# Kernel tuning notes

Measured on AMD Instinct MI355X. Metric: run time of the kernel, lower is better.

Reference implementation:

```python
import jax, jax.numpy as jnp
import numpy as np

B, F, E, A, T, H = 16384, 1024, 28, 2, 128, 4
HD = T // H  # head dim = 32

def _ln(x, g, b, eps=1e-5):
    m = jnp.mean(x, axis=-1, keepdims=True)
    v = jnp.var(x, axis=-1, keepdims=True)
    return (x - m) / jnp.sqrt(v + eps) * g + b

def _gelu(x):
    return jax.nn.gelu(x, approximate=False)  # torch nn.GELU default (erf)

def setup_inputs() -> dict:
    key = jax.random.key(0)
    ks = iter(jax.random.split(key, 48))
    def rn(shape, s=0.02):
        return jax.random.normal(next(ks), shape, jnp.float32) * s
    d = dict(
        fusion_feat=jax.random.normal(next(ks), (B, F), jnp.float32),
        explicit_logits=jax.random.normal(next(ks), (B, E), jnp.float32),
        implicit_logits=jax.random.normal(next(ks), (B, E), jnp.float32),
        affect_vec=jax.random.normal(next(ks), (B, A), jnp.float32),
        ln_exp_g=jnp.ones((E,), jnp.float32), ln_exp_b=jnp.zeros((E,), jnp.float32),
        W_exp=rn((E, T)), b_exp=jnp.zeros((T,), jnp.float32),
        ln_imp_g=jnp.ones((E,), jnp.float32), ln_imp_b=jnp.zeros((E,), jnp.float32),
        W_imp=rn((E, T)), b_imp=jnp.zeros((T,), jnp.float32),
        ln_aff_g=jnp.ones((A,), jnp.float32), ln_aff_b=jnp.zeros((A,), jnp.float32),
        W_aff=rn((A, T)), b_aff=jnp.zeros((T,), jnp.float32),
        Wq_in=rn((F, T)), bq_in=jnp.zeros((T,), jnp.float32),   # query_proj
        Wq=rn((T, T)), bq=jnp.zeros((T,), jnp.float32),         # MHA in_proj q
        Wk=rn((T, T)), bk=jnp.zeros((T,), jnp.float32),         # MHA in_proj k
        Wv=rn((T, T)), bv=jnp.zeros((T,), jnp.float32),         # MHA in_proj v
        Wo=rn((T, T)), bo=jnp.zeros((T,), jnp.float32),         # MHA out_proj
        Wc=rn((T, F)), bc=jnp.zeros((F,), jnp.float32),         # context_proj
        Ws=rn((3 * T, F)), bs=jnp.zeros((F,), jnp.float32),     # summary_proj
        Wg1=rn((2 * F, F)), bg1=jnp.zeros((F,), jnp.float32),   # gate layer 1
        Wg2=rn((F, F)), bg2=jnp.zeros((F,), jnp.float32),       # gate layer 2
        ln_out_g=jnp.ones((F,), jnp.float32), ln_out_b=jnp.zeros((F,), jnp.float32),
    )
    return d

def reference(fusion_feat, explicit_logits, implicit_logits, affect_vec,
              ln_exp_g, ln_exp_b, W_exp, b_exp,
              ln_imp_g, ln_imp_b, W_imp, b_imp,
              ln_aff_g, ln_aff_b, W_aff, b_aff,
              Wq_in, bq_in, Wq, bq, Wk, bk, Wv, bv, Wo, bo,
              Wc, bc, Ws, bs, Wg1, bg1, Wg2, bg2, ln_out_g, ln_out_b):
    p_exp = jax.nn.softmax(explicit_logits, axis=-1)
    p_imp = jax.nn.softmax(implicit_logits, axis=-1)
    exp_e = _gelu(_ln(p_exp, ln_exp_g, ln_exp_b) @ W_exp + b_exp)       # (B,T)
    imp_e = _gelu(_ln(p_imp, ln_imp_g, ln_imp_b) @ W_imp + b_imp)       # (B,T)
    aff_e = _gelu(_ln(affect_vec, ln_aff_g, ln_aff_b) @ W_aff + b_aff)  # (B,T)
    tokens = jnp.stack([exp_e, imp_e, aff_e], axis=1)                   # (B,3,T)
    q = fusion_feat @ Wq_in + bq_in                                     # (B,T)
    # tiny 1-query x 3-key multi-head cross attention (dropout=eval/identity)
    qh = (q @ Wq + bq).reshape(B, H, HD)
    kh = (tokens @ Wk + bk).reshape(B, 3, H, HD)
    vh = (tokens @ Wv + bv).reshape(B, 3, H, HD)
    scores = jnp.einsum('bhd,bshd->bhs', qh, kh) / np.float32(np.sqrt(HD))
    w = jax.nn.softmax(scores, axis=-1)                                 # (B,H,3)
    attn_weights = jnp.mean(w, axis=1)                                  # avg heads -> (B,3)
    attn_out = jnp.einsum('bhs,bshd->bhd', w, vh).reshape(B, T) @ Wo + bo
    context = attn_out @ Wc + bc                                        # (B,F)
    gate_h = _gelu(jnp.concatenate([fusion_feat, context], axis=-1) @ Wg1 + bg1)
    gate = jax.nn.sigmoid(gate_h @ Wg2 + bg2)
    refined = _ln(fusion_feat + gate * context, ln_out_g, ln_out_b)
    summary = _gelu(jnp.concatenate([exp_e, imp_e, aff_e], axis=-1) @ Ws + bs)
    return refined, attn_weights, summary
```

## Files before the change

### kernel.cpp

```cpp
#include <hip/hip_runtime.h>
#include <hip/hip_bf16.h>
#include <stdint.h>


using bf16 = __hip_bfloat16;
typedef __bf16 bf16x8 __attribute__((ext_vector_type(8)));
typedef float f32x4 __attribute__((ext_vector_type(4)));

__device__ __forceinline__ float b2f(bf16 x) { return __bfloat162float(x); }
__device__ __forceinline__ bf16 f2b(float x) { return __float2bfloat16(x); }

__device__ __forceinline__ float fast_tanh(float y) {
  float z = fabsf(y);
  float t = __expf(-2.f * z);
  float r = (1.f - t) / (1.f + t);
  return copysignf(r, y);
}
__device__ __forceinline__ float gelu_f(float x) {
  return 0.5f * x * (1.f + fast_tanh(0.7978845608028654f * (x + 0.044715f * x * x * x)));
}
__device__ __forceinline__ float sigmoid_f(float v) {
  return 1.f / (1.f + __expf(-v));
}

__device__ __forceinline__ void async_ld16(const void* g, void* l) {
  using GP = const __attribute__((address_space(1))) uint32_t*;
  using LP = __attribute__((address_space(3))) uint32_t*;
  __builtin_amdgcn_global_load_lds((GP)g, (LP)l, 16, 0, 0);
}

template <int EPI, typename OutT, int MT>
__device__ __forceinline__ void gemm128_dev(
    int bx, int by,
    const bf16* A0, const bf16* A1, int ksplit, int lda0, int lda1,
    const bf16* __restrict__ BT, int K,
    const float* __restrict__ bias,
    OutT* out, int ldo,
    const bf16* ffp, const bf16* ctxp, int ldfc)
{
  constexpr int MIC = MT / 32;
  __shared__ uint16_t smA[MT * 64];
  __shared__ uint16_t smB[128 * 64];
  const int tid = threadIdx.x;
  const int w = tid >> 6;
  const int l = tid & 63;
  const int m0 = bx * MT;
  const int n0 = by * 128;
  const int wr = w >> 1, wc = w & 1;
  const int lrow = l & 15, lquad = l >> 4;
  const int rb = w * 8 + (l >> 3);
  const int cpos = l & 7;

  const f32x4 vzero = {0.f, 0.f, 0.f, 0.f};
  f32x4 acc[MIC][4];
#pragma unroll
  for (int i = 0; i < MIC; i++)
#pragma unroll
    for (int j = 0; j < 4; j++) acc[i][j] = vzero;

  for (int k0 = 0; k0 < K; k0 += 64) {
    __syncthreads();
#pragma unroll
    for (int i = 0; i < MIC; i++) {
      int row = i * 32 + rb;
      int cg = cpos ^ (row & 7);
      int kcol = k0 + cg * 8;
      const bf16* gp = (kcol < ksplit)
                           ? (A0 + (size_t)(m0 + row) * lda0 + kcol)
                           : (A1 + (size_t)(m0 + row) * lda1 + (kcol - ksplit));
      async_ld16(gp, &smA[(i * 32 + w * 8) * 64]);
    }
#pragma unroll
    for (int i = 0; i < 4; i++) {
      int row = i * 32 + rb;
      int cg = cpos ^ (row & 7);
      const bf16* gq = BT + (size_t)(n0 + row) * K + k0 + cg * 8;
      async_ld16(gq, &smB[(i * 32 + w * 8) * 64]);
    }
    __syncthreads();
#pragma unroll
    for (int kk = 0; kk < 2; kk++) {
      bf16x8 af[MIC], bfr[4];
      const int cc = kk * 4 + lquad;
#pragma unroll
      for (int mi = 0; mi < MIC; mi++) {
        int r = wr * (MT / 2) + mi * 16 + lrow;
        af[mi] = *(const bf16x8*)&smA[r * 64 + ((cc ^ (r & 7)) << 3)];
      }
#pragma unroll
      for (int ni = 0; ni < 4; ni++) {
        int r = wc * 64 + ni * 16 + lrow;
        bfr[ni] = *(const bf16x8*)&smB[r * 64 + ((cc ^ (r & 7)) << 3)];
      }
#pragma unroll
      for (int mi = 0; mi < MIC; mi++)
#pragma unroll
        for (int ni = 0; ni < 4; ni++)
          acc[mi][ni] =
              __builtin_amdgcn_mfma_f32_16x16x32_bf16(af[mi], bfr[ni], acc[mi][ni], 0, 0, 0);
    }
  }

#pragma unroll
  for (int mi = 0; mi < MIC; mi++) {
#pragma unroll
    for (int ni = 0; ni < 4; ni++) {
#pragma unroll
      for (int r = 0; r < 4; r++) {
        int row = m0 + wr * (MT / 2) + mi * 16 + lquad * 4 + r;
        int col = n0 + wc * 64 + ni * 16 + lrow;
        float v = acc[mi][ni][r] + (bias ? bias[col] : 0.f);
        if (EPI == 1) v = gelu_f(v);
        if (EPI == 2) {
          float gate = sigmoid_f(v);
          size_t fo = (size_t)row * ldfc + col;
          v = b2f(ffp[fo]) + gate * b2f(ctxp[fo]);
        }
        if constexpr (__is_same(OutT, float))
          out[(size_t)row * ldo + col] = v;
        else
          out[(size_t)row * ldo + col] = f2b(v);
      }
    }
  }
}

template <int EPI, typename OutT>
__device__ __forceinline__ void gemm256_dev(
    uint16_t* __restrict__ smem, int bx, int by,
    const bf16* A0, const bf16* A1, int ksplit, int lda0, int lda1,
    const bf16* B0, const bf16* B1, int bsplit, int ldb0, int ldb1,
    int K,
    const float* __restrict__ bias,
    OutT* out, int ldo,
    const bf16* ffp, const bf16* ctxp, int ldfc)
{
  const int tid = threadIdx.x;
  const int w = tid >> 6;
  const int l = tid & 63;
  const int m0 = bx * 256;
  const int n0 = by * 256;
  const int wr = w >> 2;
  const int wc = w & 3;
  const int lrow = l & 15, lquad = l >> 4;
  const int rb = tid >> 3;
  const int cpos = tid & 7;
  const int NT = K >> 6;

  const f32x4 vzero = {0.f, 0.f, 0.f, 0.f};
  f32x4 acc[8][4];
#pragma unroll
  for (int mi = 0; mi < 8; mi++)
#pragma unroll
    for (int ni = 0; ni < 4; ni++) acc[mi][ni] = vzero;

  auto stage = [&](int buf, int tt) {
    const int k0 = tt << 6;
    const bf16* Ab; int la, kc;
    if (k0 < ksplit) { Ab = A0; la = lda0; kc = k0; }
    else             { Ab = A1; la = lda1; kc = k0 - ksplit; }
    uint16_t* sA = smem + buf * 16384;
#pragma unroll
    for (int i = 0; i < 4; i++) {
      const int row = i * 64 + rb;
      const int cg = cpos ^ (row & 7);
      async_ld16(Ab + (size_t)(m0 + row) * la + kc + cg * 8,
                 &sA[(i * 64 + w * 8) * 64]);
    }
    const bf16* Bb; int lb, kb;
    if (k0 < bsplit) { Bb = B0; lb = ldb0; kb = k0; }
    else             { Bb = B1; lb = ldb1; kb = k0 - bsplit; }
    uint16_t* sB = smem + 32768 + buf * 16384;
#pragma unroll
    for (int i = 0; i < 4; i++) {
      const int row = i * 64 + rb;
      const int cg = cpos ^ (row & 7);
      async_ld16(Bb + (size_t)(n0 + row) * lb + kb + cg * 8,
                 &sB[(i * 64 + w * 8) * 64]);
    }
  };

  int cur = 0;

  auto readfrags = [&](int kk, bf16x8 (&af)[8], bf16x8 (&bfr)[4]) {
    const uint16_t* sA = smem + cur * 16384;
    const uint16_t* sB = smem + 32768 + cur * 16384;
    const int cc = kk * 4 + lquad;
#pragma unroll
    for (int mi = 0; mi < 8; mi++) {
      int r = wr * 128 + mi * 16 + lrow;
      af[mi] = *(const bf16x8*)&sA[r * 64 + ((cc ^ (r & 7)) << 3)];
    }
#pragma unroll
    for (int ni = 0; ni < 4; ni++) {
      int r = wc * 64 + ni * 16 + lrow;
      bfr[ni] = *(const bf16x8*)&sB[r * 64 + ((cc ^ (r & 7)) << 3)];
    }
  };
  auto domfma = [&](bf16x8 (&af)[8], bf16x8 (&bfr)[4]) {
#pragma unroll
    for (int mi = 0; mi < 8; mi++)
#pragma unroll
      for (int ni = 0; ni < 4; ni++)
        acc[mi][ni] =
            __builtin_amdgcn_mfma_f32_16x16x32_bf16(af[mi], bfr[ni], acc[mi][ni], 0, 0, 0);
  };

  stage(0, 0);
  stage(1, 1);
  asm volatile("s_waitcnt vmcnt(8)" ::: "memory");
  __builtin_amdgcn_s_barrier();
  __builtin_amdgcn_sched_barrier(0);

  for (int t = 0; t < NT; ++t) {
    bf16x8 af[8], bfr[4];
    readfrags(0, af, bfr);
    __builtin_amdgcn_s_setprio(1);
    domfma(af, bfr);
    __builtin_amdgcn_s_setprio(0);
    readfrags(1, af, bfr);
    asm volatile("s_waitcnt lgkmcnt(0)" ::: "memory");
    __builtin_amdgcn_s_barrier();
    __builtin_amdgcn_sched_barrier(0);
    if (t + 2 < NT) stage(cur, t + 2);
    __builtin_amdgcn_s_setprio(1);
    domfma(af, bfr);
    __builtin_amdgcn_s_setprio(0);
    if (t + 2 < NT) {
      asm volatile("s_waitcnt vmcnt(8)" ::: "memory");
    } else {
      asm volatile("s_waitcnt vmcnt(0)" ::: "memory");
    }
    __builtin_amdgcn_s_barrier();
    __builtin_amdgcn_sched_barrier(0);
    cur ^= 1;
  }

#pragma unroll
  for (int mi = 0; mi < 8; mi++) {
#pragma unroll
    for (int ni = 0; ni < 4; ni++) {
#pragma unroll
      for (int r = 0; r < 4; r++) {
        int row = m0 + wr * 128 + mi * 16 + lquad * 4 + r;
        int col = n0 + wc * 64 + ni * 16 + lrow;
        float v = acc[mi][ni][r] + (bias ? bias[col] : 0.f);
        if (EPI == 1) v = gelu_f(v);
        if (EPI == 2) {
          float gate = sigmoid_f(v);
          size_t fo = (size_t)row * ldfc + col;
          v = b2f(ffp[fo]) + gate * b2f(ctxp[fo]);
        }
        if constexpr (__is_same(OutT, float))
          out[(size_t)row * ldo + col] = v;
        else
          out[(size_t)row * ldo + col] = f2b(v);
      }
    }
  }
}

__launch_bounds__(512, 2)
__global__ void big5_k(const bf16* FFB, const bf16* APRE,
                       const bf16* WG1T, const bf16* WFOLD, const float* BG1F,
                       bf16* GATEH,
                       const bf16* WOCT, const float* BOC, bf16* CTX)
{
  __shared__ uint16_t smem[65536];
  int bid = blockIdx.x;
  if (bid < 256) {
    gemm256_dev<1, bf16>(smem, bid & 63, bid >> 6,
                         FFB, APRE, 1024, 1024, 128,
                         WG1T, WFOLD, 1024, 2048, 128,
                         1152, BG1F, GATEH, 1024, nullptr, nullptr, 0);
  } else {
    bid -= 256;
    gemm256_dev<0, bf16>(smem, bid & 63, bid >> 6,
                         APRE, APRE, 128, 128, 128,
                         WOCT, WOCT, 128, 128, 128,
                         128, BOC, CTX, 1024, nullptr, nullptr, 0);
  }
}

__launch_bounds__(512, 2)
__global__ void big6_k(const bf16* GATEH, const bf16* WG2T, const float* bg2,
                       bf16* PRE, const bf16* FFB, const bf16* CTX,
                       const bf16* TOK, const bf16* WST, const float* bs, float* SUMM)
{
  __shared__ uint16_t smem[65536];
  int bid = blockIdx.x;
  if (bid < 256) {
    gemm256_dev<2, bf16>(smem, bid & 63, bid >> 6,
                         GATEH, GATEH, 1024, 1024, 1024,
                         WG2T, WG2T, 1024, 1024, 1024,
                         1024, bg2, PRE, 1024, FFB, CTX, 1024);
  } else {
    bid -= 256;
    gemm256_dev<1, float>(smem, bid & 63, bid >> 6,
                          TOK, TOK, 384, 384, 384,
                          WST, WST, 384, 384, 384,
                          384, bs, SUMM, 1024, nullptr, nullptr, 0);
  }
}

__launch_bounds__(256)
__global__ void folds_a(const bf16* WQT, const bf16* WQINB, bf16* WQQT,
                        const bf16* WCT, const bf16* WOB, bf16* WOCT, bf16* WOC,
                        const float* __restrict__ Wg1, const float* __restrict__ BOC,
                        const float* __restrict__ bg1, float* BG1F)
{
  int bid = blockIdx.x;
  if (bid < 8) {
    gemm128_dev<0, bf16, 128>(0, bid, WQT, WQT, 128, 128, 128, WQINB, 128,
                              nullptr, WQQT, 1024, nullptr, nullptr, 0);
  } else if (bid < 16) {
    gemm128_dev<0, bf16, 128>(bid - 8, 0, WCT, WCT, 128, 128, 128, WOB, 128,
                              nullptr, WOCT, 128, nullptr, nullptr, 0);
  } else if (bid < 24) {
    gemm128_dev<0, bf16, 128>(0, bid - 16, WOB, WOB, 128, 128, 128, WCT, 128,
                              nullptr, WOC, 1024, nullptr, nullptr, 0);
  } else {
    int f = (bid - 24) * 256 + threadIdx.x;
    float s = bg1[f];
    for (int c = 0; c < 1024; c++) s += BOC[c] * Wg1[(size_t)(1024 + c) * 1024 + f];
    BG1F[f] = s;
  }
}

__launch_bounds__(256)
__global__ void g12_k(const bf16* FFB, const bf16* WQQT, const float* BQQ, bf16* QH,
                      const bf16* TOK, const bf16* WKVT, const float* BKV, bf16* KVH,
                      const bf16* WG1T, const bf16* WOC, bf16* WFOLD)
{
  int bid = blockIdx.x;
  if (bid < 768) {
    gemm128_dev<0, bf16, 128>(bid % 384, bid / 384, TOK, TOK, 128, 128, 128,
                              WKVT, 128, BKV, KVH, 256, nullptr, nullptr, 0);
  } else if (bid < 896) {
    gemm128_dev<0, bf16, 128>(bid - 768, 0, FFB, FFB, 1024, 1024, 1024,
                              WQQT, 1024, BQQ, QH, 128, nullptr, nullptr, 0);
  } else {
    gemm128_dev<0, bf16, 128>(bid - 896, 0, WG1T + 1024, WG1T + 1024, 2048, 2048, 2048,
                              WOC, 1024, nullptr, WFOLD, 128, nullptr, nullptr, 0);
  }
}

__device__ __forceinline__ void emb28_256(const float* __restrict__ logits,
                                          const float* __restrict__ g,
                                          const float* __restrict__ bb,
                                          const float* __restrict__ W,
                                          const float* __restrict__ wb,
                                          bf16* __restrict__ out, int t,
                                          float* sv, float* sp)
{
  if (t < 28) sv[t] = logits[t];
  __syncthreads();
  float mx = sv[0];
#pragma unroll
  for (int e = 1; e < 28; e++) mx = fmaxf(mx, sv[e]);
  if (t < 28) sp[t] = __expf(sv[t] - mx);
  __syncthreads();
  float sum = 0.f;
#pragma unroll
  for (int e = 0; e < 28; e++) sum += sp[e];
  float inv = 1.f / sum;
  float sp2 = 0.f;
#pragma unroll
  for (int e = 0; e < 28; e++) { float p = sp[e] * inv; sp2 += p * p; }
  const float mean = 1.f / 28.f;
  float var = sp2 * (1.f / 28.f) - mean * mean;
  float rstd = rsqrtf(var + 1e-5f);
  __syncthreads();
  if (t < 28) sp[t] = (sp[t] * inv - mean) * rstd * g[t] + bb[t];
  __syncthreads();
  if (t < 128) {
    float acc = wb[t];
#pragma unroll
    for (int e = 0; e < 28; e++) acc += sp[e] * W[e * 128 + t];
    out[t] = f2b(gelu_f(acc));
  }
  __syncthreads();
}

__global__ void preamble(
    const float* __restrict__ ff, bf16* __restrict__ FFB,
    const float* __restrict__ exl, const float* __restrict__ iml, const float* __restrict__ affv,
    const float* __restrict__ geg, const float* __restrict__ geb,
    const float* __restrict__ Wex, const float* __restrict__ bex,
    const float* __restrict__ gig, const float* __restrict__ gib,
    const float* __restrict__ Wim, const float* __restrict__ bim,
    const float* __restrict__ gag, const float* __restrict__ gab,
    const float* __restrict__ Waf, const float* __restrict__ baf,
    bf16* __restrict__ TOK,
    const float* __restrict__ Wq, const float* __restrict__ Wc,
    const float* __restrict__ Ws, const float* __restrict__ Wg1,
    const float* __restrict__ Wg2,
    bf16* WQT, bf16* WCT, bf16* WST, bf16* WG1T, bf16* WG2T,
    const float* __restrict__ Wk, const float* __restrict__ bk,
    const float* __restrict__ Wv, const float* __restrict__ bv,
    const float* __restrict__ Wq_in, const float* __restrict__ bq_in,
    const float* __restrict__ bq, const float* __restrict__ Wo,
    const float* __restrict__ bo, const float* __restrict__ bc,
    bf16* WKVT, float* BKV, float* BQQ, float* BOC, bf16* WQINB, bf16* WOB)
{
  __shared__ float tile[32][33];
  __shared__ float sv[28], sp[28];
  int bid = blockIdx.x;
  const int t = threadIdx.x;

  if (bid < 16384) {
    size_t i = (size_t)bid * 1024 + (size_t)t * 4;
    float4 v = *reinterpret_cast<const float4*>(ff + i);
    ushort4 o;
    o.x = __builtin_bit_cast(unsigned short, f2b(v.x));
    o.y = __builtin_bit_cast(unsigned short, f2b(v.y));
    o.z = __builtin_bit_cast(unsigned short, f2b(v.z));
    o.w = __builtin_bit_cast(unsigned short, f2b(v.w));
    *reinterpret_cast<ushort4*>(FFB + i) = o;
    bf16* trow = TOK + (size_t)bid * 384;
    emb28_256(exl + (size_t)bid * 28, geg, geb, Wex, bex, trow, t, sv, sp);
    emb28_256(iml + (size_t)bid * 28, gig, gib, Wim, bim, trow + 128, t, sv, sp);
    if (t < 128) {
      float a0 = affv[(size_t)bid * 2 + 0];
      float a1 = affv[(size_t)bid * 2 + 1];
      float m = 0.5f * (a0 + a1);
      float d0 = a0 - m, d1 = a1 - m;
      float var = 0.5f * (d0 * d0 + d1 * d1);
      float rstd = rsqrtf(var + 1e-5f);
      float l0 = d0 * rstd * gag[0] + gab[0];
      float l1 = d1 * rstd * gag[1] + gab[1];
      float acc = baf[t] + l0 * Waf[t] + l1 * Waf[128 + t];
      trow[256 + t] = f2b(gelu_f(acc));
    }
    return;
  }
  bid -= 16384;
  if (bid < 3600) {
    const float* in; bf16* outp; int R, C, bx, by;
    if (bid < 16)                 { in = Wq;  outp = WQT;  R = 128;  C = 128;  bx = bid & 3;  by = bid >> 2; }
    else if ((bid -= 16) < 128)   { in = Wc;  outp = WCT;  R = 128;  C = 1024; bx = bid & 31; by = bid >> 5; }
    else if ((bid -= 128) < 384)  { in = Ws;  outp = WST;  R = 384;  C = 1024; bx = bid & 31; by = bid >> 5; }
    else if ((bid -= 384) < 2048) { in = Wg1; outp = WG1T; R = 2048; C = 1024; bx = bid & 31; by = bid >> 5; }
    else { bid -= 2048;             in = Wg2; outp = WG2T; R = 1024; C = 1024; bx = bid & 31; by = bid >> 5; }
    const int tx = t & 31, ty = t >> 5;
    const int c0 = bx * 32, r0 = by * 32;
#pragma unroll
    for (int i = 0; i < 4; i++) {
      int r = ty + i * 8;
      tile[r][tx] = in[(size_t)(r0 + r) * C + c0 + tx];
    }
    __syncthreads();
#pragma unroll
    for (int i = 0; i < 4; i++) {
      int c = ty + i * 8;
      outp[(size_t)(c0 + c) * R + r0 + tx] = f2b(tile[tx][c]);
    }
    return;
  }
  bid -= 3600;
  int idx = bid * 256 + t;
  if (idx < 32768) {
    int n = idx >> 7, k = idx & 127;
    WKVT[idx] = f2b((n < 128) ? Wk[k * 128 + n] : Wv[k * 128 + (n - 128)]);
    return;
  }
  idx -= 32768;
  if (idx < 256) { BKV[idx] = (idx < 128) ? bk[idx] : bv[idx - 128]; return; }
  idx -= 256;
  if (idx < 128) {
    float s = bq[idx];
    for (int u = 0; u < 128; u++) s += bq_in[u] * Wq[u * 128 + idx];
    BQQ[idx] = s;
    return;
  }
  idx -= 128;
  if (idx < 1024) {
    float s = bc[idx];
    for (int u = 0; u < 128; u++) s += bo[u] * Wc[u * 1024 + idx];
    BOC[idx] = s;
    return;
  }
  idx -= 1024;
  if (idx < 131072) { WQINB[idx] = f2b(Wq_in[idx]); return; }
  idx -= 131072;
  if (idx < 16384) { WOB[idx] = f2b(Wo[idx]); return; }
}

__global__ void attn_kernel(const bf16* __restrict__ qh, const bf16* __restrict__ kvh,
                            bf16* __restrict__ apre, float* __restrict__ attw)
{
  const int b = blockIdx.x, t = threadIdx.x;
  float q = b2f(qh[(size_t)b * 128 + t]);
  const bf16* kv = kvh + (size_t)b * 3 * 256;
  float s[3], v[3];
#pragma unroll
  for (int i = 0; i < 3; i++) {
    float k = b2f(kv[i * 256 + t]);
    v[i] = b2f(kv[i * 256 + 128 + t]);
    float r = q * k;
#pragma unroll
    for (int off = 16; off > 0; off >>= 1) r += __shfl_down(r, off, 32);
    r = __shfl(r, 0, 32);
    s[i] = r * 0.17677669529663687f;
  }
  float mx = fmaxf(s[0], fmaxf(s[1], s[2]));
  float e0 = __expf(s[0] - mx), e1 = __expf(s[1] - mx), e2 = __expf(s[2] - mx);
  float inv = 1.f / (e0 + e1 + e2);
  float w0 = e0 * inv, w1 = e1 * inv, w2 = e2 * inv;
  apre[(size_t)b * 128 + t] = f2b(w0 * v[0] + w1 * v[1] + w2 * v[2]);
  __shared__ float aw[4][3];
  if ((t & 31) == 0) { int h = t >> 5; aw[h][0] = w0; aw[h][1] = w1; aw[h][2] = w2; }
  __syncthreads();
  if (t < 3)
    attw[(size_t)b * 3 + t] = 0.25f * (aw[0][t] + aw[1][t] + aw[2][t] + aw[3][t]);
}

__global__ void ln_out_kernel(const bf16* __restrict__ x, const float* __restrict__ g,
                              const float* __restrict__ bb, float* __restrict__ out)
{
  const int row = blockIdx.x, t = threadIdx.x;
  const bf16* xr = x + (size_t)row * 1024;
  ushort4 u = *reinterpret_cast<const ushort4*>(xr + t * 4);
  float v0 = __uint_as_float((uint32_t)u.x << 16);
  float v1 = __uint_as_float((uint32_t)u.y << 16);
  float v2 = __uint_as_float((uint32_t)u.z << 16);
  float v3 = __uint_as_float((uint32_t)u.w << 16);
  float s = v0 + v1 + v2 + v3;
  float s2 = v0 * v0 + v1 * v1 + v2 * v2 + v3 * v3;
#pragma unroll
  for (int off = 32; off > 0; off >>= 1) {
    s += __shfl_down(s, off, 64);
    s2 += __shfl_down(s2, off, 64);
  }
  __shared__ float ls[4], ls2[4];
  const int w = t >> 6;
  if ((t & 63) == 0) { ls[w] = s; ls2[w] = s2; }
  __syncthreads();
  float S = ls[0] + ls[1] + ls[2] + ls[3];
  float S2 = ls2[0] + ls2[1] + ls2[2] + ls2[3];
  float mean = S * (1.f / 1024.f);
  float var = S2 * (1.f / 1024.f) - mean * mean;
  float rstd = rsqrtf(var + 1e-5f);
  const int c = t * 4;
  float4 o;
  o.x = (v0 - mean) * rstd * g[c + 0] + bb[c + 0];
  o.y = (v1 - mean) * rstd * g[c + 1] + bb[c + 1];
  o.z = (v2 - mean) * rstd * g[c + 2] + bb[c + 2];
  o.w = (v3 - mean) * rstd * g[c + 3] + bb[c + 3];
  *reinterpret_cast<float4*>(out + (size_t)row * 1024 + c) = o;
}

extern "C" void kernel_launch(void* const* d_in, const int* in_sizes, int n_in,
                              void* d_out, int out_size, void* d_ws, size_t ws_size,
                              hipStream_t stream)
{
  const float* ff   = (const float*)d_in[0];
  const float* exl  = (const float*)d_in[1];
  const float* iml  = (const float*)d_in[2];
  const float* affv = (const float*)d_in[3];
  const float* geg = (const float*)d_in[4],  *geb = (const float*)d_in[5];
  const float* Wex = (const float*)d_in[6],  *bex = (const float*)d_in[7];
  const float* gig = (const float*)d_in[8],  *gib = (const float*)d_in[9];
  const float* Wim = (const float*)d_in[10], *bim = (const float*)d_in[11];
  const float* gag = (const float*)d_in[12], *gab = (const float*)d_in[13];
  const float* Waf = (const float*)d_in[14], *baf = (const float*)d_in[15];
  const float* Wq_in = (const float*)d_in[16], *bq_in = (const float*)d_in[17];
  const float* Wq = (const float*)d_in[18], *bq = (const float*)d_in[19];
  const float* Wk = (const float*)d_in[20], *bk = (const float*)d_in[21];
  const float* Wv = (const float*)d_in[22], *bv = (const float*)d_in[23];
  const float* Wo = (const float*)d_in[24], *bo = (const float*)d_in[25];
  const float* Wc = (const float*)d_in[26], *bc = (const float*)d_in[27];
  const float* Ws = (const float*)d_in[28], *bs = (const float*)d_in[29];
  const float* Wg1 = (const float*)d_in[30], *bg1 = (const float*)d_in[31];
  const float* Wg2 = (const float*)d_in[32], *bg2 = (const float*)d_in[33];
  const float* lng = (const float*)d_in[34], *lnb = (const float*)d_in[35];

  char* ws = (char*)d_ws;
  bf16*  WKVT = (bf16*)(ws + 0);
  float* BKV  = (float*)(ws + 65536);
  bf16*  WQQT = (bf16*)(ws + 66560);
  float* BQQ  = (float*)(ws + 328704);
  bf16*  WOCT = (bf16*)(ws + 329216);
  float* BOC  = (float*)(ws + 591360);
  bf16*  WST  = (bf16*)(ws + 595456);
  bf16*  WG1T = (bf16*)(ws + 1381888);
  bf16*  WG2T = (bf16*)(ws + 5576192);
  bf16*  FFB  = (bf16*)(ws + 7673344);
  bf16*  PRE  = (bf16*)(ws + 7673344);
  bf16*  TOK  = (bf16*)(ws + 41227776);
  bf16*  QH   = (bf16*)(ws + 53810688);
  bf16*  APRE = (bf16*)(ws + 58004992);

  bf16* WQT   = (bf16*)(ws + 53810688);
  bf16* WOB   = (bf16*)(ws + 53810688 + 32768);
  bf16* WQINB = (bf16*)(ws + 53810688 + 65536);
  bf16* WCT   = (bf16*)(ws + 53810688 + 327680);

  float* outp = (float*)d_out;
  float* out_refined = outp;
  float* out_attw    = outp + 16777216;
  float* out_summary = outp + 16826368;
  bf16* CTX   = (bf16*)out_refined;
  bf16* GATEH = (bf16*)((char*)out_refined + 33554432);
  bf16* KVH   = (bf16*)out_summary;
  bf16* WOC   = (bf16*)((char*)out_summary + 33554432);
  bf16* WFOLD = (bf16*)((char*)out_summary + 34603008);
  float* BG1F = (float*)((char*)out_summary + 35127296);

  preamble<<<20694, 256, 0, stream>>>(
      ff, FFB, exl, iml, affv, geg, geb, Wex, bex, gig, gib, Wim, bim,
      gag, gab, Waf, baf, TOK,
      Wq, Wc, Ws, Wg1, Wg2, WQT, WCT, WST, WG1T, WG2T,
      Wk, bk, Wv, bv, Wq_in, bq_in, bq, Wo, bo, bc,
      WKVT, BKV, BQQ, BOC, WQINB, WOB);
  folds_a<<<28, 256, 0, stream>>>(WQT, WQINB, WQQT, WCT, WOB, WOCT, WOC,
                                  Wg1, BOC, bg1, BG1F);
  g12_k<<<904, 256, 0, stream>>>(FFB, WQQT, BQQ, QH, TOK, WKVT, BKV, KVH,
                                 WG1T, WOC, WFOLD);
  attn_kernel<<<16384, 128, 0, stream>>>(QH, KVH, APRE, out_attw);
  big5_k<<<512, 512, 0, stream>>>(FFB, APRE, WG1T, WFOLD, BG1F, GATEH,
                                  WOCT, BOC, CTX);
  big6_k<<<512, 512, 0, stream>>>(GATEH, WG2T, bg2, PRE, FFB, CTX,
                                  TOK, WST, bs, out_summary);
  ln_out_kernel<<<16384, 256, 0, stream>>>(PRE, lng, lnb, out_refined);
}
```

Baseline: 576.3 us.

## Split fused multi-GEMM kernels into separate per-GEMM launches

Separates the combined preamble into a per-row activation kernel and a weight-transposition kernel. It also splits the two merged GEMM kernels into four dedicated launches, with the small context projection using a 128-tile GEMM. The intent is to avoid mixing blocks with very different amounts of work in one grid, which causes load imbalance. The cost is extra kernel launches and lost overlap between independent GEMMs.

```diff
diff --git a/kernel.cpp b/kernel.cpp
--- a/kernel.cpp
+++ b/kernel.cpp
@@ -260,47 +260,44 @@
   }
 }
 
+__launch_bounds__(256)
+__global__ void g3_k(const bf16* APRE, const bf16* WOCT, const float* BOC, bf16* CTX)
+{
+  gemm128_dev<0, bf16, 128>(blockIdx.x, blockIdx.y, APRE, APRE, 128, 128, 128,
+                            WOCT, 128, BOC, CTX, 1024, nullptr, nullptr, 0);
+}
+
 __launch_bounds__(512, 2)
-__global__ void big5_k(const bf16* FFB, const bf16* APRE,
-                       const bf16* WG1T, const bf16* WFOLD, const float* BG1F,
-                       bf16* GATEH,
-                       const bf16* WOCT, const float* BOC, bf16* CTX)
+__global__ void g5_k(const bf16* FFB, const bf16* APRE,
+                     const bf16* WG1T, const bf16* WFOLD, const float* BG1F,
+                     bf16* GATEH)
 {
   __shared__ uint16_t smem[65536];
-  int bid = blockIdx.x;
-  if (bid < 256) {
-    gemm256_dev<1, bf16>(smem, bid & 63, bid >> 6,
-                         FFB, APRE, 1024, 1024, 128,
-                         WG1T, WFOLD, 1024, 2048, 128,
-                         1152, BG1F, GATEH, 1024, nullptr, nullptr, 0);
-  } else {
-    bid -= 256;
-    gemm256_dev<0, bf16>(smem, bid & 63, bid >> 6,
-                         APRE, APRE, 128, 128, 128,
-                         WOCT, WOCT, 128, 128, 128,
-                         128, BOC, CTX, 1024, nullptr, nullptr, 0);
-  }
+  gemm256_dev<1, bf16>(smem, blockIdx.x & 63, blockIdx.x >> 6,
+                       FFB, APRE, 1024, 1024, 128,
+                       WG1T, WFOLD, 1024, 2048, 128,
+                       1152, BG1F, GATEH, 1024, nullptr, nullptr, 0);
 }
 
 __launch_bounds__(512, 2)
-__global__ void big6_k(const bf16* GATEH, const bf16* WG2T, const float* bg2,
-                       bf16* PRE, const bf16* FFB, const bf16* CTX,
-                       const bf16* TOK, const bf16* WST, const float* bs, float* SUMM)
+__global__ void g6_k(const bf16* GATEH, const bf16* WG2T, const float* bg2,
+                     bf16* PRE, const bf16* FFB, const bf16* CTX)
 {
   __shared__ uint16_t smem[65536];
-  int bid = blockIdx.x;
-  if (bid < 256) {
-    gemm256_dev<2, bf16>(smem, bid & 63, bid >> 6,
-                         GATEH, GATEH, 1024, 1024, 1024,
-                         WG2T, WG2T, 1024, 1024, 1024,
-                         1024, bg2, PRE, 1024, FFB, CTX, 1024);
-  } else {
-    bid -= 256;
-    gemm256_dev<1, float>(smem, bid & 63, bid >> 6,
-                          TOK, TOK, 384, 384, 384,
-                          WST, WST, 384, 384, 384,
-                          384, bs, SUMM, 1024, nullptr, nullptr, 0);
-  }
+  gemm256_dev<2, bf16>(smem, blockIdx.x & 63, blockIdx.x >> 6,
+                       GATEH, GATEH, 1024, 1024, 1024,
+                       WG2T, WG2T, 1024, 1024, 1024,
+                       1024, bg2, PRE, 1024, FFB, CTX, 1024);
+}
+
+__launch_bounds__(512, 2)
+__global__ void g4_k(const bf16* TOK, const bf16* WST, const float* bs, float* SUMM)
+{
+  __shared__ uint16_t smem[65536];
+  gemm256_dev<1, float>(smem, blockIdx.x & 63, blockIdx.x >> 6,
+                        TOK, TOK, 384, 384, 384,
+                        WST, WST, 384, 384, 384,
+                        384, bs, SUMM, 1024, nullptr, nullptr, 0);
 }
 
 __launch_bounds__(256)
@@ -382,7 +379,7 @@
   __syncthreads();
 }
 
-__global__ void preamble(
+__global__ void pre_rows(
     const float* __restrict__ ff, bf16* __restrict__ FFB,
     const float* __restrict__ exl, const float* __restrict__ iml, const float* __restrict__ affv,
     const float* __restrict__ geg, const float* __restrict__ geb,
@@ -391,7 +388,36 @@
     const float* __restrict__ Wim, const float* __restrict__ bim,
     const float* __restrict__ gag, const float* __restrict__ gab,
     const float* __restrict__ Waf, const float* __restrict__ baf,
-    bf16* __restrict__ TOK,
+    bf16* __restrict__ TOK)
+{
+  __shared__ float sv[28], sp[28];
+  const int b = blockIdx.x, t = threadIdx.x;
+  size_t i = (size_t)b * 1024 + (size_t)t * 4;
+  float4 v = *reinterpret_cast<const float4*>(ff + i);
+  ushort4 o;
+  o.x = __builtin_bit_cast(unsigned short, f2b(v.x));
+  o.y = __builtin_bit_cast(unsigned short, f2b(v.y));
+  o.z = __builtin_bit_cast(unsigned short, f2b(v.z));
+  o.w = __builtin_bit_cast(unsigned short, f2b(v.w));
+  *reinterpret_cast<ushort4*>(FFB + i) = o;
+  bf16* trow = TOK + (size_t)b * 384;
+  emb28_256(exl + (size_t)b * 28, geg, geb, Wex, bex, trow, t, sv, sp);
+  emb28_256(iml + (size_t)b * 28, gig, gib, Wim, bim, trow + 128, t, sv, sp);
+  if (t < 128) {
+    float a0 = affv[(size_t)b * 2 + 0];
+    float a1 = affv[(size_t)b * 2 + 1];
+    float m = 0.5f * (a0 + a1);
+    float d0 = a0 - m, d1 = a1 - m;
+    float var = 0.5f * (d0 * d0 + d1 * d1);
+    float rstd = rsqrtf(var + 1e-5f);
+    float l0 = d0 * rstd * gag[0] + gab[0];
+    float l1 = d1 * rstd * gag[1] + gab[1];
+    float acc = baf[t] + l0 * Waf[t] + l1 * Waf[128 + t];
+    trow[256 + t] = f2b(gelu_f(acc));
+  }
+}
+
+__global__ void pre_w(
     const float* __restrict__ Wq, const float* __restrict__ Wc,
     const float* __restrict__ Ws, const float* __restrict__ Wg1,
     const float* __restrict__ Wg2,
@@ -404,37 +430,8 @@
     bf16* WKVT, float* BKV, float* BQQ, float* BOC, bf16* WQINB, bf16* WOB)
 {
   __shared__ float tile[32][33];
-  __shared__ float sv[28], sp[28];
   int bid = blockIdx.x;
   const int t = threadIdx.x;
-
-  if (bid < 16384) {
-    size_t i = (size_t)bid * 1024 + (size_t)t * 4;
-    float4 v = *reinterpret_cast<const float4*>(ff + i);
-    ushort4 o;
-    o.x = __builtin_bit_cast(unsigned short, f2b(v.x));
-    o.y = __builtin_bit_cast(unsigned short, f2b(v.y));
-    o.z = __builtin_bit_cast(unsigned short, f2b(v.z));
-    o.w = __builtin_bit_cast(unsigned short, f2b(v.w));
-    *reinterpret_cast<ushort4*>(FFB + i) = o;
-    bf16* trow = TOK + (size_t)bid * 384;
-    emb28_256(exl + (size_t)bid * 28, geg, geb, Wex, bex, trow, t, sv, sp);
-    emb28_256(iml + (size_t)bid * 28, gig, gib, Wim, bim, trow + 128, t, sv, sp);
-    if (t < 128) {
-      float a0 = affv[(size_t)bid * 2 + 0];
-      float a1 = affv[(size_t)bid * 2 + 1];
-      float m = 0.5f * (a0 + a1);
-      float d0 = a0 - m, d1 = a1 - m;
-      float var = 0.5f * (d0 * d0 + d1 * d1);
-      float rstd = rsqrtf(var + 1e-5f);
-      float l0 = d0 * rstd * gag[0] + gab[0];
-      float l1 = d1 * rstd * gag[1] + gab[1];
-      float acc = baf[t] + l0 * Waf[t] + l1 * Waf[128 + t];
-      trow[256 + t] = f2b(gelu_f(acc));
-    }
-    return;
-  }
-  bid -= 16384;
   if (bid < 3600) {
     const float* in; bf16* outp; int R, C, bx, by;
     if (bid < 16)                 { in = Wq;  outp = WQT;  R = 128;  C = 128;  bx = bid & 3;  by = bid >> 2; }
@@ -607,20 +604,19 @@
   bf16* WFOLD = (bf16*)((char*)out_summary + 34603008);
   float* BG1F = (float*)((char*)out_summary + 35127296);
 
-  preamble<<<20694, 256, 0, stream>>>(
-      ff, FFB, exl, iml, affv, geg, geb, Wex, bex, gig, gib, Wim, bim,
-      gag, gab, Waf, baf, TOK,
-      Wq, Wc, Ws, Wg1, Wg2, WQT, WCT, WST, WG1T, WG2T,
-      Wk, bk, Wv, bv, Wq_in, bq_in, bq, Wo, bo, bc,
-      WKVT, BKV, BQQ, BOC, WQINB, WOB);
+  pre_rows<<<16384, 256, 0, stream>>>(ff, FFB, exl, iml, affv, geg, geb, Wex, bex,
+                                      gig, gib, Wim, bim, gag, gab, Waf, baf, TOK);
+  pre_w<<<4310, 256, 0, stream>>>(Wq, Wc, Ws, Wg1, Wg2, WQT, WCT, WST, WG1T, WG2T,
+                                  Wk, bk, Wv, bv, Wq_in, bq_in, bq, Wo, bo, bc,
+                                  WKVT, BKV, BQQ, BOC, WQINB, WOB);
   folds_a<<<28, 256, 0, stream>>>(WQT, WQINB, WQQT, WCT, WOB, WOCT, WOC,
                                   Wg1, BOC, bg1, BG1F);
   g12_k<<<904, 256, 0, stream>>>(FFB, WQQT, BQQ, QH, TOK, WKVT, BKV, KVH,
                                  WG1T, WOC, WFOLD);
   attn_kernel<<<16384, 128, 0, stream>>>(QH, KVH, APRE, out_attw);
-  big5_k<<<512, 512, 0, stream>>>(FFB, APRE, WG1T, WFOLD, BG1F, GATEH,
-                                  WOCT, BOC, CTX);
-  big6_k<<<512, 512, 0, stream>>>(GATEH, WG2T, bg2, PRE, FFB, CTX,
-                                  TOK, WST, bs, out_summary);
+  g3_k<<<dim3(128, 8), 256, 0, stream>>>(APRE, WOCT, BOC, CTX);
+  g5_k<<<256, 512, 0, stream>>>(FFB, APRE, WG1T, WFOLD, BG1F, GATEH);
+  g6_k<<<256, 512, 0, stream>>>(GATEH, WG2T, bg2, PRE, FFB, CTX);
+  g4_k<<<256, 512, 0, stream>>>(TOK, WST, bs, out_summary);
   ln_out_kernel<<<16384, 256, 0, stream>>>(PRE, lng, lnb, out_refined);
 }
```

Result: slower. 591.2 us (+2.6%).
